# Kernel optimization log

Measured on AMD Instinct MI355X. Metric: run time of the kernel, lower is better.

## Reference

```python
import jax, jax.numpy as jnp
import numpy as np
import math

B, T, E, H = 64, 256, 1024, 16
HD = E // H  # 64
EPS = 1e-5


def layernorm(x, g, b):
    mu = jnp.mean(x, axis=-1, keepdims=True)
    var = jnp.mean(jnp.square(x - mu), axis=-1, keepdims=True)
    return (x - mu) * jax.lax.rsqrt(var + EPS) * g + b


def setup_inputs() -> dict:
    key = jax.random.key(0)
    ks = jax.random.split(key, 10)
    s = 0.02
    return {
        "x": jax.random.normal(ks[0], (B, T, E), dtype=jnp.float32),
        "ln1_g": jnp.ones((E,), jnp.float32),
        "ln1_b": jnp.zeros((E,), jnp.float32),
        "wk": jax.random.normal(ks[1], (H, E, HD), jnp.float32) * s,
        "wq": jax.random.normal(ks[2], (H, E, HD), jnp.float32) * s,
        "wv": jax.random.normal(ks[3], (H, E, HD), jnp.float32) * s,
        "w_proj": jax.random.normal(ks[4], (E, E), jnp.float32) * s,
        "b_proj": jnp.zeros((E,), jnp.float32),
        "ln2_g": jnp.ones((E,), jnp.float32),
        "ln2_b": jnp.zeros((E,), jnp.float32),
        "w1": jax.random.normal(ks[5], (E, E), jnp.float32) * s,
        "b1": jnp.zeros((E,), jnp.float32),
        "w2": jax.random.normal(ks[6], (E, E), jnp.float32) * s,
        "b2": jnp.zeros((E,), jnp.float32),
    }


def reference(x, ln1_g, ln1_b, wk, wq, wv, w_proj, b_proj, ln2_g, ln2_b, w1, b1, w2, b2):
    # --- multi-head causal attention on LN1(x) ---
    h = layernorm(x, ln1_g, ln1_b)
    k = jnp.einsum('bte,hed->bhtd', h, wk)
    q = jnp.einsum('bte,hed->bhtd', h, wq)
    v = jnp.einsum('bte,hed->bhtd', h, wv)
    # NOTE: original computes k @ q^T (K.Q^T), not the standard Q.K^T -- kept faithful
    scores = jnp.einsum('bhtd,bhsd->bhts', k, q) / math.sqrt(HD)
    mask = jnp.tril(jnp.ones((T, T), dtype=bool))
    scores = jnp.where(mask, scores, -jnp.inf)
    attn_w = jax.nn.softmax(scores, axis=-1)  # dropout = identity in eval
    attn = jnp.einsum('bhts,bhsd->bhtd', attn_w, v)
    attn = attn.transpose(0, 2, 1, 3).reshape(B, T, E)  # concat heads
    x = x + attn @ w_proj + b_proj
    # --- feed-forward on LN2(x) ---
    h2 = layernorm(x, ln2_g, ln2_b)
    ff = jax.nn.relu(h2 @ w1 + b1) @ w2 + b2
    return x + ff
```

## Files before the change

kernel.cpp:

```cpp
#include <hip/hip_runtime.h>

typedef unsigned int u32;
typedef unsigned short u16;
typedef __attribute__((ext_vector_type(8))) short bf16x8;
typedef __attribute__((ext_vector_type(4))) float f32x4;

#define GLOBAL_AS __attribute__((address_space(1)))
#define LDS_AS    __attribute__((address_space(3)))

#define B_   64
#define T_   256
#define E_   1024
#define H_   16
#define HD_  64
#define NTOK (B_*T_)
#define K_   1024
#define LNEPS 1e-5f

__device__ __forceinline__ float bflo(u32 u){ return __uint_as_float(u << 16); }
__device__ __forceinline__ float bfhi(u32 u){ return __uint_as_float(u & 0xffff0000u); }
__device__ __forceinline__ u16 f2bf(float f){
  u32 x = __float_as_uint(f);
  u32 r = x + 0x7fffu + ((x >> 16) & 1u);
  return (u16)(r >> 16);
}
__device__ __forceinline__ u16 f2bf_trunc(float f){
  return (u16)(__float_as_uint(f) >> 16);
}
__device__ __forceinline__ u32 pack2(float a, float b){
  return (u32)f2bf(a) | ((u32)f2bf(b) << 16);
}

__device__ __forceinline__ void gload16(const u16* g, u16* l){
  __builtin_amdgcn_global_load_lds((const GLOBAL_AS void*)g, (LDS_AS void*)l, 16, 0, 0);
}

__global__ __launch_bounds__(256) void ln_bf16_kernel(
    const float* __restrict__ x, const float* __restrict__ g,
    const float* __restrict__ b, u16* __restrict__ o)
{
  int lane  = threadIdx.x & 63;
  int token = (blockIdx.x << 2) + (threadIdx.x >> 6);
  const float4* xr = (const float4*)(x + (size_t)token * E_);
  float4 v[4];
  float s = 0.f, ss = 0.f;
  #pragma unroll
  for (int i = 0; i < 4; ++i){
    v[i] = xr[lane + 64 * i];
    s += v[i].x + v[i].y + v[i].z + v[i].w;
    ss = fmaf(v[i].x, v[i].x, fmaf(v[i].y, v[i].y,
         fmaf(v[i].z, v[i].z, fmaf(v[i].w, v[i].w, ss))));
  }
  #pragma unroll
  for (int off = 32; off > 0; off >>= 1){
    s  += __shfl_xor(s,  off);
    ss += __shfl_xor(ss, off);
  }
  float mu   = s * (1.f / E_);
  float var  = ss * (1.f / E_) - mu * mu;
  float rstd = rsqrtf(var + LNEPS);
  const float4* gr = (const float4*)g;
  const float4* br = (const float4*)b;
  uint2* orow = (uint2*)(o + (size_t)token * E_);
  #pragma unroll
  for (int i = 0; i < 4; ++i){
    float4 gg = gr[lane + 64 * i], bb = br[lane + 64 * i];
    float y0 = (v[i].x - mu) * rstd * gg.x + bb.x;
    float y1 = (v[i].y - mu) * rstd * gg.y + bb.y;
    float y2 = (v[i].z - mu) * rstd * gg.z + bb.z;
    float y3 = (v[i].w - mu) * rstd * gg.w + bb.w;
    orow[lane + 64 * i] = make_uint2(pack2(y0, y1), pack2(y2, y3));
  }
}

__global__ __launch_bounds__(256) void convq_kernel(
    const float* __restrict__ wk, const float* __restrict__ wq,
    const float* __restrict__ wv, u16* __restrict__ o)
{
  __shared__ float tile[64 * 68];
  const int zh = blockIdx.x, z = zh >> 4, h = zh & 15;
  const int e0 = blockIdx.y << 6;
  const float* w = (z == 0 ? wk : z == 1 ? wq : wv) + (size_t)h * (E_ * HD_);
  const int t = threadIdx.x;
  {
    int er = t >> 2, d0 = (t & 3) << 4;
    const float4* src = (const float4*)(w + (size_t)(e0 + er) * HD_ + d0);
    #pragma unroll
    for (int i = 0; i < 4; ++i)
      *(float4*)(tile + er * 68 + d0 + 4 * i) = src[i];
  }
  __syncthreads();
  {
    int dr = t >> 2, ee = (t & 3) << 4;
    u32 wd[8];
    #pragma unroll
    for (int j = 0; j < 8; ++j)
      wd[j] = pack2(tile[(ee + 2*j) * 68 + dr], tile[(ee + 2*j + 1) * 68 + dr]);
    u16* dst = o + (size_t)(z * 1024 + h * 64 + dr) * K_ + e0 + ee;
    *(uint4*)(dst    ) = make_uint4(wd[0], wd[1], wd[2], wd[3]);
    *(uint4*)(dst + 8) = make_uint4(wd[4], wd[5], wd[6], wd[7]);
  }
}

__global__ __launch_bounds__(256) void convt_kernel(
    const float* __restrict__ w, u16* __restrict__ o)
{
  __shared__ float tile[64 * 68];
  const int n0 = blockIdx.x << 6, k0 = blockIdx.y << 6;
  const int t = threadIdx.x;
  {
    int kr = t >> 2, nn = (t & 3) << 4;
    const float4* src = (const float4*)(w + (size_t)(k0 + kr) * E_ + n0 + nn);
    #pragma unroll
    for (int i = 0; i < 4; ++i)
      *(float4*)(tile + kr * 68 + nn + 4 * i) = src[i];
  }
  __syncthreads();
  {
    int nr = t >> 2, kk = (t & 3) << 4;
    u32 wd[8];
    #pragma unroll
    for (int j = 0; j < 8; ++j)
      wd[j] = pack2(tile[(kk + 2*j) * 68 + nr], tile[(kk + 2*j + 1) * 68 + nr]);
    u16* dst = o + (size_t)(n0 + nr) * K_ + k0 + kk;
    *(uint4*)(dst    ) = make_uint4(wd[0], wd[1], wd[2], wd[3]);
    *(uint4*)(dst + 8) = make_uint4(wd[4], wd[5], wd[6], wd[7]);
  }
}

template<int MODE>
__global__ __launch_bounds__(256) void mgemm_kernel(
    const u16* __restrict__ A, const u16* __restrict__ Bt,
    const float* __restrict__ bias, const float* __restrict__ resid,
    float* __restrict__ Cf, u16* __restrict__ Cb, u16* __restrict__ Cb2)
{
  __shared__ __align__(16) u16 lds[16384];
  u16* As = lds;
  u16* Bs = lds + 8192;
  const int row0 = blockIdx.x * 128, col0 = blockIdx.y * 128;
  const int tid = threadIdx.x, lane = tid & 63;
  const int wv_ = tid >> 6, wm = wv_ >> 1, wn = wv_ & 1;
  const int l15 = lane & 15, quad = lane >> 4;

  const int srow   = tid >> 3;
  const int schunk = ((tid & 7) ^ ((tid >> 3) & 7)) << 3;
  const u16* Ag = A  + (size_t)(row0 + srow) * K_ + schunk;
  const u16* Bg = Bt + (size_t)(col0 + srow) * K_ + schunk;
  u16* Ald = As + tid * 8;
  u16* Bld = Bs + tid * 8;

  f32x4 acc[4][4];
  #pragma unroll
  for (int i = 0; i < 4; ++i)
    #pragma unroll
    for (int j = 0; j < 4; ++j)
      acc[i][j] = (f32x4){0.f, 0.f, 0.f, 0.f};

  const int mrow = wm * 64, nrow = wn * 64;
  for (int k0 = 0; k0 < K_; k0 += 64) {
    __syncthreads();
    #pragma unroll
    for (int p = 0; p < 4; ++p) {
      gload16(Ag + (size_t)(p * 32) * K_ + k0, Ald + p * 2048);
      gload16(Bg + (size_t)(p * 32) * K_ + k0, Bld + p * 2048);
    }
    __syncthreads();
    #pragma unroll
    for (int ss = 0; ss < 2; ++ss) {
      bf16x8 a[4], b[4];
      #pragma unroll
      for (int i = 0; i < 4; ++i){
        int ma = mrow + i * 16 + l15, nb = nrow + i * 16 + l15;
        a[i] = *(const bf16x8*)(As + ma * 64 + ((((ss << 2) | quad)) ^ (ma & 7)) * 8);
        b[i] = *(const bf16x8*)(Bs + nb * 64 + ((((ss << 2) | quad)) ^ (nb & 7)) * 8);
      }
      #pragma unroll
      for (int i = 0; i < 4; ++i)
        #pragma unroll
        for (int j = 0; j < 4; ++j)
          acc[i][j] = __builtin_amdgcn_mfma_f32_16x16x32_bf16(a[i], b[j], acc[i][j], 0, 0, 0);
    }
  }

  if (MODE == 1 || MODE == 3) {
    #pragma unroll
    for (int j = 0; j < 4; ++j) {
      const int n = col0 + wn * 64 + j * 16 + l15;
      float bn = bias[n];
      #pragma unroll
      for (int i = 0; i < 4; ++i)
        #pragma unroll
        for (int r = 0; r < 4; ++r) {
          const int row = row0 + wm * 64 + i * 16 + quad * 4 + r;
          size_t idx = (size_t)row * E_ + n;
          float v = acc[i][j][r] + bn;
          if (MODE == 1) Cf[idx] = v + resid[idx];
          else           Cf[idx] = v + Cf[idx];
        }
    }
    return;
  }

  __syncthreads();
  u16* ep = lds + wv_ * 4096;
  const int nb0 = col0 + wn * 64;

  if (MODE == 2) {
    #pragma unroll
    for (int j = 0; j < 4; ++j) {
      float bn = bias[nb0 + j * 16 + l15];
      #pragma unroll
      for (int i = 0; i < 4; ++i)
        #pragma unroll
        for (int r = 0; r < 4; ++r)
          ep[(i*16 + quad*4 + r) * 64 + j*16 + l15] =
              f2bf(fmaxf(acc[i][j][r] + bn, 0.f));
    }
    __syncthreads();
    const int rbase = row0 + wm * 64;
    #pragma unroll
    for (int it = 0; it < 8; ++it) {
      int tl = it * 8 + (lane >> 3), c = lane & 7;
      uint4 v = *(const uint4*)(ep + tl * 64 + c * 8);
      *(uint4*)(Cb + (size_t)(rbase + tl) * E_ + nb0 + c * 8) = v;
    }
    return;
  }

  const int z = nb0 >> 10, h = (nb0 >> 6) & 15;
  const int bb = (row0 + wm * 64) >> 8, tb0 = (row0 + wm * 64) & 255;
  if (z < 2) {
    #pragma unroll
    for (int i = 0; i < 4; ++i)
      #pragma unroll
      for (int j = 0; j < 4; ++j)
        #pragma unroll
        for (int r = 0; r < 4; ++r)
          ep[(i*16 + quad*4 + r) * 64 + j*16 + l15] = f2bf(acc[i][j][r]);
  } else {
    #pragma unroll
    for (int i = 0; i < 4; ++i)
      #pragma unroll
      for (int j = 0; j < 4; ++j)
        #pragma unroll
        for (int r = 0; r < 4; ++r) {
          int tl = i*16 + quad*4 + r, d = j*16 + l15;
          int cs = (tl >> 3) ^ (d & 7);
          ep[d * 64 + cs * 8 + (tl & 7)] = f2bf(acc[i][j][r]);
        }
  }
  __syncthreads();
  if (z < 2) {
    u16* out = (z == 0 ? Cb : Cb2) + ((size_t)(bb * H_ + h) * T_ + tb0) * HD_;
    #pragma unroll
    for (int it = 0; it < 8; ++it) {
      int tl = it * 8 + (lane >> 3), c = lane & 7;
      uint4 v = *(const uint4*)(ep + tl * 64 + c * 8);
      *(uint4*)(out + (size_t)tl * HD_ + c * 8) = v;
    }
  } else {
    u16* out = (u16*)Cf + ((size_t)(bb * H_ + h) * HD_) * T_;
    #pragma unroll
    for (int it = 0; it < 8; ++it) {
      int dl = it * 8 + (lane >> 3), c = lane & 7;
      int cs = c ^ (dl & 7);
      uint4 v = *(const uint4*)(ep + dl * 64 + cs * 8);
      *(uint4*)(out + (size_t)dl * T_ + tb0 + c * 8) = v;
    }
  }
}

__global__ __launch_bounds__(256) void fattn_kernel(
    const u16* __restrict__ kk_, const u16* __restrict__ qq_,
    const u16* __restrict__ vt_, u16* __restrict__ out)
{
  __shared__ __align__(16) u16 Pb[4][64 * 72];
  const int tid = threadIdx.x, lane = tid & 63, wv = tid >> 6;
  const int bh = blockIdx.x * 4 + wv;
  const int tblk = blockIdx.y;
  const int l15 = lane & 15, quad = lane >> 4;
  const u16* kb  = kk_ + (size_t)bh * (T_ * HD_);
  const u16* qb  = qq_ + (size_t)bh * (T_ * HD_);
  const u16* vtb = vt_ + (size_t)bh * (HD_ * T_);
  u16* Pw = Pb[wv];

  bf16x8 kf[4][2];
  #pragma unroll
  for (int i = 0; i < 4; ++i)
    #pragma unroll
    for (int c = 0; c < 2; ++c)
      kf[i][c] = *(const bf16x8*)(kb + (size_t)(tblk*64 + i*16 + l15) * HD_ + c*32 + quad*8);

  f32x4 o[4][4];
  float mrow[4][4], lrow[4][4];
  #pragma unroll
  for (int i = 0; i < 4; ++i) {
    #pragma unroll
    for (int j = 0; j < 4; ++j) o[i][j] = (f32x4){0.f, 0.f, 0.f, 0.f};
    #pragma unroll
    for (int r = 0; r < 4; ++r) { mrow[i][r] = -1e30f; lrow[i][r] = 0.f; }
  }

  for (int sb = 0; sb <= tblk; ++sb) {
    f32x4 S[4][4];
    #pragma unroll
    for (int j = 0; j < 4; ++j) {
      bf16x8 qf0 = *(const bf16x8*)(qb + (size_t)(sb*64 + j*16 + l15) * HD_ +      quad*8);
      bf16x8 qf1 = *(const bf16x8*)(qb + (size_t)(sb*64 + j*16 + l15) * HD_ + 32 + quad*8);
      #pragma unroll
      for (int i = 0; i < 4; ++i) {
        f32x4 t0 = __builtin_amdgcn_mfma_f32_16x16x32_bf16(kf[i][0], qf0,
                       (f32x4){0.f,0.f,0.f,0.f}, 0, 0, 0);
        S[i][j] = __builtin_amdgcn_mfma_f32_16x16x32_bf16(kf[i][1], qf1, t0, 0, 0, 0);
      }
    }
    #pragma unroll
    for (int i = 0; i < 4; ++i)
      #pragma unroll
      for (int j = 0; j < 4; ++j)
        #pragma unroll
        for (int r = 0; r < 4; ++r) {
          float val = S[i][j][r] * 0.125f;
          if (sb == tblk) {
            int tl = i*16 + quad*4 + r, sl = j*16 + l15;
            if (sl > tl) val = -1e30f;
          }
          S[i][j][r] = val;
        }
    #pragma unroll
    for (int i = 0; i < 4; ++i)
      #pragma unroll
      for (int r = 0; r < 4; ++r) {
        float mx = fmaxf(fmaxf(S[i][0][r], S[i][1][r]), fmaxf(S[i][2][r], S[i][3][r]));
        #pragma unroll
        for (int msk = 1; msk < 16; msk <<= 1) mx = fmaxf(mx, __shfl_xor(mx, msk));
        float mn = fmaxf(mrow[i][r], mx);
        float al = __expf(mrow[i][r] - mn);
        mrow[i][r] = mn;
        float sm = 0.f;
        #pragma unroll
        for (int j = 0; j < 4; ++j) {
          float p = __expf(S[i][j][r] - mn);
          S[i][j][r] = p;
          sm += p;
        }
        #pragma unroll
        for (int msk = 1; msk < 16; msk <<= 1) sm += __shfl_xor(sm, msk);
        lrow[i][r] = lrow[i][r] * al + sm;
        #pragma unroll
        for (int jd = 0; jd < 4; ++jd) o[i][jd][r] *= al;
      }
    #pragma unroll
    for (int i = 0; i < 4; ++i)
      #pragma unroll
      for (int j = 0; j < 4; ++j)
        #pragma unroll
        for (int r = 0; r < 4; ++r)
          Pw[(i*16 + quad*4 + r) * 72 + j*16 + l15] = f2bf_trunc(S[i][j][r]);
    __syncthreads();
    bf16x8 pf[4][2];
    #pragma unroll
    for (int i = 0; i < 4; ++i)
      #pragma unroll
      for (int c = 0; c < 2; ++c)
        pf[i][c] = *(const bf16x8*)(Pw + (i*16 + l15) * 72 + c*32 + quad*8);
    #pragma unroll
    for (int jd = 0; jd < 4; ++jd) {
      bf16x8 vf0 = *(const bf16x8*)(vtb + (size_t)(jd*16 + l15) * T_ + sb*64 +      quad*8);
      bf16x8 vf1 = *(const bf16x8*)(vtb + (size_t)(jd*16 + l15) * T_ + sb*64 + 32 + quad*8);
      #pragma unroll
      for (int i = 0; i < 4; ++i) {
        f32x4 t0 = __builtin_amdgcn_mfma_f32_16x16x32_bf16(pf[i][0], vf0, o[i][jd], 0, 0, 0);
        o[i][jd] = __builtin_amdgcn_mfma_f32_16x16x32_bf16(pf[i][1], vf1, t0, 0, 0, 0);
      }
    }
    __syncthreads();
  }

  #pragma unroll
  for (int i = 0; i < 4; ++i)
    #pragma unroll
    for (int r = 0; r < 4; ++r) {
      float inv = 1.0f / lrow[i][r];
      #pragma unroll
      for (int jd = 0; jd < 4; ++jd)
        Pw[(i*16 + quad*4 + r) * 72 + jd*16 + l15] = f2bf(o[i][jd][r] * inv);
    }
  __syncthreads();
  {
    const int b = bh >> 4, h = bh & 15;
    const uint4* pr = (const uint4*)(Pw + lane * 72);
    uint4* og = (uint4*)(out + ((size_t)(b * T_ + tblk*64 + lane)) * E_ + h * HD_);
    #pragma unroll
    for (int k = 0; k < 8; ++k) og[k] = pr[k];
  }
}

extern "C" void kernel_launch(void* const* d_in, const int* in_sizes, int n_in,
                              void* d_out, int out_size, void* d_ws, size_t ws_size,
                              hipStream_t stream) {
  const float* x     = (const float*)d_in[0];
  const float* ln1g  = (const float*)d_in[1];
  const float* ln1b  = (const float*)d_in[2];
  const float* wk    = (const float*)d_in[3];
  const float* wq    = (const float*)d_in[4];
  const float* wv    = (const float*)d_in[5];
  const float* wproj = (const float*)d_in[6];
  const float* bproj = (const float*)d_in[7];
  const float* ln2g  = (const float*)d_in[8];
  const float* ln2b  = (const float*)d_in[9];
  const float* w1    = (const float*)d_in[10];
  const float* b1    = (const float*)d_in[11];
  const float* w2    = (const float*)d_in[12];
  const float* b2    = (const float*)d_in[13];
  float* outp = (float*)d_out;

  char* ws = (char*)d_ws;
  const size_t MB = 1024 * 1024;
  u16* wqkvT  = (u16*)(ws);
  u16* wprojT = (u16*)(ws + 6 * MB);
  u16* w1T    = (u16*)(ws + 8 * MB);
  u16* w2T    = (u16*)(ws + 10 * MB);
  u16* hb     = (u16*)(ws + 16 * MB);
  u16* kbuf   = (u16*)(ws + 48 * MB);
  u16* qbuf   = (u16*)(ws + 80 * MB);
  u16* vtbuf  = (u16*)d_out;

  convq_kernel<<<dim3(48, 16), 256, 0, stream>>>(wk, wq, wv, wqkvT);
  convt_kernel<<<dim3(16, 16), 256, 0, stream>>>(wproj, wprojT);
  convt_kernel<<<dim3(16, 16), 256, 0, stream>>>(w1, w1T);
  convt_kernel<<<dim3(16, 16), 256, 0, stream>>>(w2, w2T);

  ln_bf16_kernel<<<NTOK/4, 256, 0, stream>>>(x, ln1g, ln1b, hb);
  mgemm_kernel<0><<<dim3(NTOK/128, 3*E_/128), 256, 0, stream>>>(
      hb, wqkvT, nullptr, nullptr, (float*)vtbuf, kbuf, qbuf);
  fattn_kernel<<<dim3(B_*H_/4, 4), 256, 0, stream>>>(kbuf, qbuf, vtbuf, hb);
  mgemm_kernel<1><<<dim3(NTOK/128, E_/128), 256, 0, stream>>>(
      hb, wprojT, bproj, x, outp, nullptr, nullptr);
  ln_bf16_kernel<<<NTOK/4, 256, 0, stream>>>(outp, ln2g, ln2b, kbuf);
  mgemm_kernel<2><<<dim3(NTOK/128, E_/128), 256, 0, stream>>>(
      kbuf, w1T, b1, nullptr, nullptr, qbuf, nullptr);
  mgemm_kernel<3><<<dim3(NTOK/128, E_/128), 256, 0, stream>>>(
      qbuf, w2T, b2, nullptr, outp, nullptr, nullptr);
}
```

Baseline: 523.1 us.

## Merge prep kernels, store residual stream in bf16, swap grid axes for GEMMs

Folds the four weight-conversion kernels and the first layernorm into one prep launch. The post-attention residual x1 becomes a bf16 buffer written through the LDS epilogue, replacing an fp32 store. LN2 and the final GEMM read it as bf16, and the final GEMM no longer read-modify-writes fp32 output. GEMM grids swap x/y so blocks sharing a row panel run together for better L2 reuse of A, at the cost of lower precision in the residual stream.

Measured after the change: 525.9 us. About the same (+0.5%).

```diff
diff --git a/kernel.cpp b/kernel.cpp
--- a/kernel.cpp
+++ b/kernel.cpp
@@ -17,8 +17,7 @@
 #define K_   1024
 #define LNEPS 1e-5f
 
-__device__ __forceinline__ float bflo(u32 u){ return __uint_as_float(u << 16); }
-__device__ __forceinline__ float bfhi(u32 u){ return __uint_as_float(u & 0xffff0000u); }
+__device__ __forceinline__ float bf2f(u16 u){ return __uint_as_float(((u32)u) << 16); }
 __device__ __forceinline__ u16 f2bf(float f){
   u32 x = __float_as_uint(f);
   u32 r = x + 0x7fffu + ((x >> 16) & 1u);
@@ -35,22 +34,119 @@
   __builtin_amdgcn_global_load_lds((const GLOBAL_AS void*)g, (LDS_AS void*)l, 16, 0, 0);
 }
 
-__global__ __launch_bounds__(256) void ln_bf16_kernel(
-    const float* __restrict__ x, const float* __restrict__ g,
+__global__ __launch_bounds__(256) void prep_kernel(
+    const float* __restrict__ wk, const float* __restrict__ wq,
+    const float* __restrict__ wv, const float* __restrict__ wproj,
+    const float* __restrict__ w1, const float* __restrict__ w2,
+    const float* __restrict__ x, const float* __restrict__ g1,
+    const float* __restrict__ be1,
+    u16* __restrict__ wqkvT, u16* __restrict__ wprojT,
+    u16* __restrict__ w1T, u16* __restrict__ w2T, u16* __restrict__ hb)
+{
+  __shared__ float tile[64 * 68];
+  const int bid = blockIdx.x, t = threadIdx.x;
+  if (bid < 768) {
+    const int zh = bid >> 4, z = zh >> 4, h = zh & 15;
+    const int e0 = (bid & 15) << 6;
+    const float* w = (z == 0 ? wk : z == 1 ? wq : wv) + (size_t)h * (E_ * HD_);
+    {
+      int er = t >> 2, d0 = (t & 3) << 4;
+      const float4* src = (const float4*)(w + (size_t)(e0 + er) * HD_ + d0);
+      #pragma unroll
+      for (int i = 0; i < 4; ++i)
+        *(float4*)(tile + er * 68 + d0 + 4 * i) = src[i];
+    }
+    __syncthreads();
+    {
+      int dr = t >> 2, ee = (t & 3) << 4;
+      u32 wd[8];
+      #pragma unroll
+      for (int j = 0; j < 8; ++j)
+        wd[j] = pack2(tile[(ee + 2*j) * 68 + dr], tile[(ee + 2*j + 1) * 68 + dr]);
+      u16* dst = wqkvT + (size_t)(z * 1024 + h * 64 + dr) * K_ + e0 + ee;
+      *(uint4*)(dst    ) = make_uint4(wd[0], wd[1], wd[2], wd[3]);
+      *(uint4*)(dst + 8) = make_uint4(wd[4], wd[5], wd[6], wd[7]);
+    }
+  } else if (bid < 1536) {
+    const int r = bid - 768, wsel = r >> 8, within = r & 255;
+    const float* w = (wsel == 0 ? wproj : wsel == 1 ? w1 : w2);
+    u16* o = (wsel == 0 ? wprojT : wsel == 1 ? w1T : w2T);
+    const int n0 = (within & 15) << 6, k0 = (within >> 4) << 6;
+    {
+      int kr = t >> 2, nn = (t & 3) << 4;
+      const float4* src = (const float4*)(w + (size_t)(k0 + kr) * E_ + n0 + nn);
+      #pragma unroll
+      for (int i = 0; i < 4; ++i)
+        *(float4*)(tile + kr * 68 + nn + 4 * i) = src[i];
+    }
+    __syncthreads();
+    {
+      int nr = t >> 2, kk = (t & 3) << 4;
+      u32 wd[8];
+      #pragma unroll
+      for (int j = 0; j < 8; ++j)
+        wd[j] = pack2(tile[(kk + 2*j) * 68 + nr], tile[(kk + 2*j + 1) * 68 + nr]);
+      u16* dst = o + (size_t)(n0 + nr) * K_ + k0 + kk;
+      *(uint4*)(dst    ) = make_uint4(wd[0], wd[1], wd[2], wd[3]);
+      *(uint4*)(dst + 8) = make_uint4(wd[4], wd[5], wd[6], wd[7]);
+    }
+  } else {
+    int lane  = t & 63;
+    int token = ((bid - 1536) << 2) + (t >> 6);
+    const float4* xr = (const float4*)(x + (size_t)token * E_);
+    float4 v[4];
+    float s = 0.f, ss = 0.f;
+    #pragma unroll
+    for (int i = 0; i < 4; ++i){
+      v[i] = xr[lane + 64 * i];
+      s += v[i].x + v[i].y + v[i].z + v[i].w;
+      ss = fmaf(v[i].x, v[i].x, fmaf(v[i].y, v[i].y,
+           fmaf(v[i].z, v[i].z, fmaf(v[i].w, v[i].w, ss))));
+    }
+    #pragma unroll
+    for (int off = 32; off > 0; off >>= 1){
+      s  += __shfl_xor(s,  off);
+      ss += __shfl_xor(ss, off);
+    }
+    float mu   = s * (1.f / E_);
+    float var  = ss * (1.f / E_) - mu * mu;
+    float rstd = rsqrtf(var + LNEPS);
+    const float4* gr = (const float4*)g1;
+    const float4* br = (const float4*)be1;
+    uint2* orow = (uint2*)(hb + (size_t)token * E_);
+    #pragma unroll
+    for (int i = 0; i < 4; ++i){
+      float4 gg = gr[lane + 64 * i], bb = br[lane + 64 * i];
+      float y0 = (v[i].x - mu) * rstd * gg.x + bb.x;
+      float y1 = (v[i].y - mu) * rstd * gg.y + bb.y;
+      float y2 = (v[i].z - mu) * rstd * gg.z + bb.z;
+      float y3 = (v[i].w - mu) * rstd * gg.w + bb.w;
+      orow[lane + 64 * i] = make_uint2(pack2(y0, y1), pack2(y2, y3));
+    }
+  }
+}
+
+__global__ __launch_bounds__(256) void ln2_kernel(
+    const u16* __restrict__ x1, const float* __restrict__ g,
     const float* __restrict__ b, u16* __restrict__ o)
 {
   int lane  = threadIdx.x & 63;
   int token = (blockIdx.x << 2) + (threadIdx.x >> 6);
-  const float4* xr = (const float4*)(x + (size_t)token * E_);
-  float4 v[4];
+  const uint4* xr = (const uint4*)(x1 + (size_t)token * E_);
+  float f[16];
   float s = 0.f, ss = 0.f;
   #pragma unroll
-  for (int i = 0; i < 4; ++i){
-    v[i] = xr[lane + 64 * i];
-    s += v[i].x + v[i].y + v[i].z + v[i].w;
-    ss = fmaf(v[i].x, v[i].x, fmaf(v[i].y, v[i].y,
-         fmaf(v[i].z, v[i].z, fmaf(v[i].w, v[i].w, ss))));
-  }
+  for (int i = 0; i < 2; ++i){
+    uint4 u = xr[lane * 2 + i];
+    u32 w[4] = {u.x, u.y, u.z, u.w};
+    #pragma unroll
+    for (int j = 0; j < 4; ++j){
+      f[i*8 + 2*j    ] = __uint_as_float(w[j] << 16);
+      f[i*8 + 2*j + 1] = __uint_as_float(w[j] & 0xffff0000u);
+    }
+  }
+  #pragma unroll
+  for (int j = 0; j < 16; ++j){ s += f[j]; ss = fmaf(f[j], f[j], ss); }
   #pragma unroll
   for (int off = 32; off > 0; off >>= 1){
     s  += __shfl_xor(s,  off);
@@ -61,83 +157,33 @@
   float rstd = rsqrtf(var + LNEPS);
   const float4* gr = (const float4*)g;
   const float4* br = (const float4*)b;
-  uint2* orow = (uint2*)(o + (size_t)token * E_);
+  u32 wd[8];
   #pragma unroll
   for (int i = 0; i < 4; ++i){
-    float4 gg = gr[lane + 64 * i], bb = br[lane + 64 * i];
-    float y0 = (v[i].x - mu) * rstd * gg.x + bb.x;
-    float y1 = (v[i].y - mu) * rstd * gg.y + bb.y;
-    float y2 = (v[i].z - mu) * rstd * gg.z + bb.z;
-    float y3 = (v[i].w - mu) * rstd * gg.w + bb.w;
-    orow[lane + 64 * i] = make_uint2(pack2(y0, y1), pack2(y2, y3));
-  }
-}
-
-__global__ __launch_bounds__(256) void convq_kernel(
-    const float* __restrict__ wk, const float* __restrict__ wq,
-    const float* __restrict__ wv, u16* __restrict__ o)
-{
-  __shared__ float tile[64 * 68];
-  const int zh = blockIdx.x, z = zh >> 4, h = zh & 15;
-  const int e0 = blockIdx.y << 6;
-  const float* w = (z == 0 ? wk : z == 1 ? wq : wv) + (size_t)h * (E_ * HD_);
-  const int t = threadIdx.x;
-  {
-    int er = t >> 2, d0 = (t & 3) << 4;
-    const float4* src = (const float4*)(w + (size_t)(e0 + er) * HD_ + d0);
-    #pragma unroll
-    for (int i = 0; i < 4; ++i)
-      *(float4*)(tile + er * 68 + d0 + 4 * i) = src[i];
-  }
-  __syncthreads();
-  {
-    int dr = t >> 2, ee = (t & 3) << 4;
-    u32 wd[8];
-    #pragma unroll
-    for (int j = 0; j < 8; ++j)
-      wd[j] = pack2(tile[(ee + 2*j) * 68 + dr], tile[(ee + 2*j + 1) * 68 + dr]);
-    u16* dst = o + (size_t)(z * 1024 + h * 64 + dr) * K_ + e0 + ee;
-    *(uint4*)(dst    ) = make_uint4(wd[0], wd[1], wd[2], wd[3]);
-    *(uint4*)(dst + 8) = make_uint4(wd[4], wd[5], wd[6], wd[7]);
-  }
-}
-
-__global__ __launch_bounds__(256) void convt_kernel(
-    const float* __restrict__ w, u16* __restrict__ o)
-{
-  __shared__ float tile[64 * 68];
-  const int n0 = blockIdx.x << 6, k0 = blockIdx.y << 6;
-  const int t = threadIdx.x;
-  {
-    int kr = t >> 2, nn = (t & 3) << 4;
-    const float4* src = (const float4*)(w + (size_t)(k0 + kr) * E_ + n0 + nn);
-    #pragma unroll
-    for (int i = 0; i < 4; ++i)
-      *(float4*)(tile + kr * 68 + nn + 4 * i) = src[i];
-  }
-  __syncthreads();
-  {
-    int nr = t >> 2, kk = (t & 3) << 4;
-    u32 wd[8];
-    #pragma unroll
-    for (int j = 0; j < 8; ++j)
-      wd[j] = pack2(tile[(kk + 2*j) * 68 + nr], tile[(kk + 2*j + 1) * 68 + nr]);
-    u16* dst = o + (size_t)(n0 + nr) * K_ + k0 + kk;
-    *(uint4*)(dst    ) = make_uint4(wd[0], wd[1], wd[2], wd[3]);
-    *(uint4*)(dst + 8) = make_uint4(wd[4], wd[5], wd[6], wd[7]);
-  }
+    float4 gg = gr[lane * 4 + i], bb = br[lane * 4 + i];
+    float y0 = (f[4*i    ] - mu) * rstd * gg.x + bb.x;
+    float y1 = (f[4*i + 1] - mu) * rstd * gg.y + bb.y;
+    float y2 = (f[4*i + 2] - mu) * rstd * gg.z + bb.z;
+    float y3 = (f[4*i + 3] - mu) * rstd * gg.w + bb.w;
+    wd[2*i]   = pack2(y0, y1);
+    wd[2*i+1] = pack2(y2, y3);
+  }
+  uint4* orow = (uint4*)(o + (size_t)token * E_ + lane * 16);
+  orow[0] = make_uint4(wd[0], wd[1], wd[2], wd[3]);
+  orow[1] = make_uint4(wd[4], wd[5], wd[6], wd[7]);
 }
 
 template<int MODE>
 __global__ __launch_bounds__(256) void mgemm_kernel(
     const u16* __restrict__ A, const u16* __restrict__ Bt,
-    const float* __restrict__ bias, const float* __restrict__ resid,
+    const float* __restrict__ bias, const float* __restrict__ residf,
+    const u16* __restrict__ residb,
     float* __restrict__ Cf, u16* __restrict__ Cb, u16* __restrict__ Cb2)
 {
   __shared__ __align__(16) u16 lds[16384];
   u16* As = lds;
   u16* Bs = lds + 8192;
-  const int row0 = blockIdx.x * 128, col0 = blockIdx.y * 128;
+  const int row0 = blockIdx.y * 128, col0 = blockIdx.x * 128;
   const int tid = threadIdx.x, lane = tid & 63;
   const int wv_ = tid >> 6, wm = wv_ >> 1, wn = wv_ & 1;
   const int l15 = lane & 15, quad = lane >> 4;
@@ -182,7 +228,7 @@
     }
   }
 
-  if (MODE == 1 || MODE == 3) {
+  if (MODE == 3) {
     #pragma unroll
     for (int j = 0; j < 4; ++j) {
       const int n = col0 + wn * 64 + j * 16 + l15;
@@ -193,9 +239,7 @@
         for (int r = 0; r < 4; ++r) {
           const int row = row0 + wm * 64 + i * 16 + quad * 4 + r;
           size_t idx = (size_t)row * E_ + n;
-          float v = acc[i][j][r] + bn;
-          if (MODE == 1) Cf[idx] = v + resid[idx];
-          else           Cf[idx] = v + Cf[idx];
+          Cf[idx] = acc[i][j][r] + bn + bf2f(residb[idx]);
         }
     }
     return;
@@ -205,16 +249,23 @@
   u16* ep = lds + wv_ * 4096;
   const int nb0 = col0 + wn * 64;
 
-  if (MODE == 2) {
+  if (MODE == 1 || MODE == 2) {
     #pragma unroll
     for (int j = 0; j < 4; ++j) {
       float bn = bias[nb0 + j * 16 + l15];
       #pragma unroll
       for (int i = 0; i < 4; ++i)
         #pragma unroll
-        for (int r = 0; r < 4; ++r)
-          ep[(i*16 + quad*4 + r) * 64 + j*16 + l15] =
-              f2bf(fmaxf(acc[i][j][r] + bn, 0.f));
+        for (int r = 0; r < 4; ++r) {
+          float v = acc[i][j][r] + bn;
+          if (MODE == 1) {
+            const int row = row0 + wm * 64 + i * 16 + quad * 4 + r;
+            v += residf[(size_t)row * E_ + nb0 + j * 16 + l15];
+          } else {
+            v = fmaxf(v, 0.f);
+          }
+          ep[(i*16 + quad*4 + r) * 64 + j*16 + l15] = f2bf(v);
+        }
     }
     __syncthreads();
     const int rbase = row0 + wm * 64;
@@ -426,20 +477,17 @@
   u16* qbuf   = (u16*)(ws + 80 * MB);
   u16* vtbuf  = (u16*)d_out;
 
-  convq_kernel<<<dim3(48, 16), 256, 0, stream>>>(wk, wq, wv, wqkvT);
-  convt_kernel<<<dim3(16, 16), 256, 0, stream>>>(wproj, wprojT);
-  convt_kernel<<<dim3(16, 16), 256, 0, stream>>>(w1, w1T);
-  convt_kernel<<<dim3(16, 16), 256, 0, stream>>>(w2, w2T);
-
-  ln_bf16_kernel<<<NTOK/4, 256, 0, stream>>>(x, ln1g, ln1b, hb);
-  mgemm_kernel<0><<<dim3(NTOK/128, 3*E_/128), 256, 0, stream>>>(
-      hb, wqkvT, nullptr, nullptr, (float*)vtbuf, kbuf, qbuf);
+  prep_kernel<<<5632, 256, 0, stream>>>(wk, wq, wv, wproj, w1, w2,
+                                        x, ln1g, ln1b,
+                                        wqkvT, wprojT, w1T, w2T, hb);
+  mgemm_kernel<0><<<dim3(3*E_/128, NTOK/128), 256, 0, stream>>>(
+      hb, wqkvT, nullptr, nullptr, nullptr, (float*)vtbuf, kbuf, qbuf);
   fattn_kernel<<<dim3(B_*H_/4, 4), 256, 0, stream>>>(kbuf, qbuf, vtbuf, hb);
-  mgemm_kernel<1><<<dim3(NTOK/128, E_/128), 256, 0, stream>>>(
-      hb, wprojT, bproj, x, outp, nullptr, nullptr);
-  ln_bf16_kernel<<<NTOK/4, 256, 0, stream>>>(outp, ln2g, ln2b, kbuf);
-  mgemm_kernel<2><<<dim3(NTOK/128, E_/128), 256, 0, stream>>>(
-      kbuf, w1T, b1, nullptr, nullptr, qbuf, nullptr);
-  mgemm_kernel<3><<<dim3(NTOK/128, E_/128), 256, 0, stream>>>(
-      qbuf, w2T, b2, nullptr, outp, nullptr, nullptr);
-}
+  mgemm_kernel<1><<<dim3(E_/128, NTOK/128), 256, 0, stream>>>(
+      hb, wprojT, bproj, x, nullptr, nullptr, kbuf, nullptr);
+  ln2_kernel<<<NTOK/4, 256, 0, stream>>>(kbuf, ln2g, ln2b, qbuf);
+  mgemm_kernel<2><<<dim3(E_/128, NTOK/128), 256, 0, stream>>>(
+      qbuf, w1T, b1, nullptr, nullptr, nullptr, hb, nullptr);
+  mgemm_kernel<3><<<dim3(E_/128, NTOK/128), 256, 0, stream>>>(
+      hb, w2T, b2, nullptr, kbuf, outp, nullptr, nullptr);
+}
```
